# Optimization experiments

Measured on AMD Instinct MI355X. Metric: run time of the kernel, lower is better.

Reference implementation:

```python
import jax, jax.numpy as jnp
import numpy as np

IN_F, OUT_F, USER_F = 1024, 512, 512
BSZ, S = 64, 256


def setup_inputs() -> dict:
    key = jax.random.key(0)
    k = jax.random.split(key, 7)
    X_doc = jax.random.normal(k[0], (BSZ, S, IN_F), dtype=jnp.float32)
    X_user = jax.random.normal(k[1], (BSZ, S, USER_F), dtype=jnp.float32)
    # xavier-normal-ish scaling for weights
    Wd = jax.random.normal(k[2], (OUT_F, IN_F), dtype=jnp.float32) * np.sqrt(2.0 / (IN_F + OUT_F))
    bd = jnp.zeros((OUT_F,), dtype=jnp.float32)
    Wu = jax.random.normal(k[3], (OUT_F, USER_F), dtype=jnp.float32) * np.sqrt(2.0 / (USER_F + OUT_F))
    bu = jnp.zeros((OUT_F,), dtype=jnp.float32)
    W = jax.random.normal(k[4], (OUT_F, OUT_F), dtype=jnp.float32) * np.sqrt(1.0 / OUT_F)
    return {"X_doc": X_doc, "X_user": X_user, "Wd": Wd, "bd": bd, "Wu": Wu, "bu": bu, "W": W}


def reference(X_doc, X_user, Wd, bd, Wu, bu, W):
    d = jnp.einsum('bsi,oi->bso', X_doc, Wd) + bd          # (b, s, out)
    u = jnp.einsum('bsi,oi->bso', X_user, Wu) + bu          # (b, s, out)
    d = d * jax.nn.sigmoid(u)
    u = u * jax.nn.sigmoid(d)
    att = jnp.tanh(jnp.einsum('bsd,de,bre->bsr', d, W, u))  # (b, s, s)
    score_d = jax.nn.softmax(att.mean(axis=2), axis=1)[..., None]  # (b, s, 1)
    score_u = jax.nn.softmax(att.mean(axis=1), axis=1)[..., None]  # (b, s, 1)
    attention_d = jnp.sum(score_d * d, axis=1)              # (b, out)
    attention_u = jnp.sum(score_u * u, axis=1)              # (b, out)
    return (attention_d, attention_u)
```

## Files before the change

kernel.cpp:

```cpp
#include <hip/hip_runtime.h>
#include <hip/hip_bf16.h>

#define S_ 256
#define BSZ_ 64
#define IN_F_ 1024
#define OUT_F_ 512
#define USER_F_ 512

typedef short short8 __attribute__((ext_vector_type(8)));
typedef float f32x4 __attribute__((ext_vector_type(4)));

__device__ __forceinline__ ushort f2bf(float f) {
  unsigned u = __float_as_uint(f);
  unsigned r = (u + 0x7FFFu + ((u >> 16) & 1u)) >> 16;
  return (ushort)r;
}
__device__ __forceinline__ float bf2f(unsigned hi16) {
  return __uint_as_float(hi16 << 16);
}
__device__ __forceinline__ float sigf(float x) {
  return 1.f / (1.f + __expf(-x));
}
__device__ __forceinline__ float tanh_safe(float x) {
  float ax = fabsf(x);
  float e = __expf(-2.f * ax);
  float r = (1.f - e) / (1.f + e);
  return copysignf(r, x);
}

__device__ __forceinline__ void gl_lds16(const ushort* g, ushort* l) {
  __builtin_amdgcn_global_load_lds(
      (const __attribute__((address_space(1))) void*)g,
      (__attribute__((address_space(3))) void*)l, 16, 0, 0);
}

__global__ void prep(const float* __restrict__ Xd, const float* __restrict__ Xu,
                     const float* __restrict__ Wd, const float* __restrict__ Wu,
                     const float* __restrict__ W,
                     ushort* __restrict__ Xd_bf, ushort* __restrict__ Xu_bf,
                     ushort* __restrict__ Wd_bf, ushort* __restrict__ Wu_bf,
                     ushort* __restrict__ Wt_bf, float* __restrict__ rowlog) {
  int i = blockIdx.x * 256 + threadIdx.x;
  if (i < 4194304) {
    float4 v = ((const float4*)Xd)[i];
    ushort4 o; o.x = f2bf(v.x); o.y = f2bf(v.y); o.z = f2bf(v.z); o.w = f2bf(v.w);
    ((ushort4*)Xd_bf)[i] = o;
  } else if (i < 6291456) {
    int j = i - 4194304;
    float4 v = ((const float4*)Xu)[j];
    ushort4 o; o.x = f2bf(v.x); o.y = f2bf(v.y); o.z = f2bf(v.z); o.w = f2bf(v.w);
    ((ushort4*)Xu_bf)[j] = o;
  } else if (i < 6422528) {
    int j = i - 6291456;
    float4 v = ((const float4*)Wd)[j];
    ushort4 o; o.x = f2bf(v.x); o.y = f2bf(v.y); o.z = f2bf(v.z); o.w = f2bf(v.w);
    ((ushort4*)Wd_bf)[j] = o;
  } else if (i < 6488064) {
    int j = i - 6422528;
    float4 v = ((const float4*)Wu)[j];
    ushort4 o; o.x = f2bf(v.x); o.y = f2bf(v.y); o.z = f2bf(v.z); o.w = f2bf(v.w);
    ((ushort4*)Wu_bf)[j] = o;
  } else if (i < 6750208) {
    int j = i - 6488064;
    Wt_bf[j] = f2bf(W[(j & 511) * 512 + (j >> 9)]);
  } else {
    int j = i - 6750208;
    ((float4*)rowlog)[j] = float4{0.f, 0.f, 0.f, 0.f};
  }
}

template <int ROWS>
__device__ __forceinline__ void stage_tile(const ushort* __restrict__ g, int K,
                                           ushort* lds, int w, int lane) {
  const int rin = lane >> 3;
  const int c = lane & 7;
#pragma unroll
  for (int i = 0; i < ROWS / 32; ++i) {
    int r = w * (ROWS / 4) + i * 8 + rin;
    int gc = c ^ (r & 7);
    gl_lds16(g + (long)r * K + gc * 8, lds + w * (ROWS / 4) * 64 + i * 512);
  }
}
__device__ __forceinline__ void stage_tile32(const ushort* __restrict__ g, int K,
                                             ushort* lds, int w, int lane) {
  const int rin = lane >> 3, c = lane & 7;
  int r = w * 8 + rin;
  int gc = c ^ (r & 7);
  gl_lds16(g + (long)r * K + gc * 8, lds + w * 512);
}

__device__ __forceinline__ short8 frag(const ushort* lds, int row, int kk, int q) {
  int pc = (kk * 4 + q) ^ (row & 7);
  return *(const short8*)(lds + row * 64 + pc * 8);
}
__device__ __forceinline__ short8 frag512(const ushort* lds, int row, int k,
                                          int kk, int q) {
  int pc = (kk * 4 + q) ^ (row & 7);
  return *(const short8*)(lds + row * 512 + k * 64 + pc * 8);
}

__device__ __forceinline__ void compute_step(const ushort* As, const ushort* Bs,
                                             f32x4 acc[2][4], int wr, int wc,
                                             int mlane, int q) {
#pragma unroll
  for (int kk = 0; kk < 2; ++kk) {
    short8 af[2], bfr[4];
#pragma unroll
    for (int r = 0; r < 2; ++r) af[r] = frag(As, wr * 32 + r * 16 + mlane, kk, q);
#pragma unroll
    for (int c = 0; c < 4; ++c) bfr[c] = frag(Bs, wc * 64 + c * 16 + mlane, kk, q);
#pragma unroll
    for (int r = 0; r < 2; ++r)
#pragma unroll
      for (int c = 0; c < 4; ++c)
        acc[r][c] = __builtin_amdgcn_mfma_f32_16x16x32_bf16(af[r], bfr[c], acc[r][c], 0, 0, 0);
  }
}

template <int NSTEP>
__device__ __forceinline__ void gemm_loop(const ushort* __restrict__ A,
                                          const ushort* __restrict__ B, int K,
                                          ushort* As, ushort* Bs, f32x4 acc[2][4],
                                          int w, int lane, int wr, int wc,
                                          int mlane, int q) {
#pragma unroll 1
  for (int k = 0; k < NSTEP; ++k) {
    stage_tile<64>(A + k * 64, K, As, w, lane);
    stage_tile<128>(B + k * 64, K, Bs, w, lane);
    __syncthreads();
    compute_step(As, Bs, acc, wr, wc, mlane, q);
    __syncthreads();
  }
}

#define ACC_ZERO(a)                             \
  _Pragma("unroll") for (int r = 0; r < 2; ++r) \
  _Pragma("unroll") for (int c = 0; c < 4; ++c) { \
    a[r][c][0] = 0.f; a[r][c][1] = 0.f; a[r][c][2] = 0.f; a[r][c][3] = 0.f; }

__global__ __launch_bounds__(256, 4) void gemm_du(
    const ushort* __restrict__ Xd, const ushort* __restrict__ Wd,
    const float* __restrict__ bd,
    const ushort* __restrict__ Xu, const ushort* __restrict__ Wu,
    const float* __restrict__ bu,
    ushort* __restrict__ dg, ushort* __restrict__ ug) {
  __shared__ ushort sm[12288];
  ushort* As = sm; ushort* Bs = sm + 4096;
  const int i = blockIdx.x;
  const int k8 = i & 7, j = i >> 3;
  const int by = k8 * 32 + (j >> 2), bx = j & 3;
  const int tid = threadIdx.x, lane = tid & 63, w = tid >> 6;
  const int wr = w >> 1, wc = w & 1, mlane = lane & 15, q = lane >> 4;
  const int m0 = by * 64, n0 = bx * 128;

  f32x4 accd[2][4]; ACC_ZERO(accd);
  gemm_loop<16>(Xd + (long)m0 * 1024, Wd + (long)n0 * 1024, 1024,
                As, Bs, accd, w, lane, wr, wc, mlane, q);
  f32x4 accu[2][4]; ACC_ZERO(accu);
  gemm_loop<8>(Xu + (long)m0 * 512, Wu + (long)n0 * 512, 512,
               As, Bs, accu, w, lane, wr, wc, mlane, q);

#pragma unroll
  for (int c = 0; c < 4; ++c) {
    const int gn = n0 + wc * 64 + c * 16 + mlane;
    const float bdv = bd[gn], buv = bu[gn];
#pragma unroll
    for (int r = 0; r < 2; ++r)
#pragma unroll
      for (int ii = 0; ii < 4; ++ii) {
        const int gm = m0 + wr * 32 + r * 16 + q * 4 + ii;
        const long idx = (long)gm * OUT_F_ + gn;
        float dp = accd[r][c][ii] + bdv;
        float up = accu[r][c][ii] + buv;
        float dgv = dp * sigf(up);
        float ugv = up * sigf(dgv);
        dg[idx] = f2bf(dgv);
        ug[idx] = f2bf(ugv);
      }
  }
}

__global__ __launch_bounds__(256, 2) void gemm_tatt(
    const ushort* __restrict__ dg, const ushort* __restrict__ Wt,
    const ushort* __restrict__ ug, float* __restrict__ rowlog,
    float* __restrict__ collog) {
  __shared__ ushort sm[32768];
  ushort* t_lds = sm;
  ushort* AsT = sm + 16384;
  ushort* BsT = sm + 18432;
  ushort* BsU = sm + 16384;
  const int i = blockIdx.x;
  const int xcd = i & 7, j = i >> 3;
  const int b = xcd * 8 + (j >> 3);
  const int by = j & 7;
  const int tid = threadIdx.x, lane = tid & 63, w = tid >> 6;
  const int mlane = lane & 15, q = lane >> 4;
  const ushort* dgs = dg + (long)b * (S_ * OUT_F_) + (long)by * 32 * 512;
  const ushort* ugb = ug + (long)b * (S_ * OUT_F_);

#pragma unroll 1
  for (int nc = 0; nc < 4; ++nc) {
    f32x4 acc[2][2];
#pragma unroll
    for (int r = 0; r < 2; ++r)
#pragma unroll
      for (int c = 0; c < 2; ++c) {
        acc[r][c][0] = 0.f; acc[r][c][1] = 0.f; acc[r][c][2] = 0.f; acc[r][c][3] = 0.f;
      }
    const ushort* Bw = Wt + (long)(nc * 128) * 512;
#pragma unroll 1
    for (int k = 0; k < 8; ++k) {
      stage_tile32(dgs + k * 64, 512, AsT, w, lane);
      stage_tile<128>(Bw + k * 64, 512, BsT, w, lane);
      __syncthreads();
#pragma unroll
      for (int kk = 0; kk < 2; ++kk) {
        short8 af[2], bfr[2];
#pragma unroll
        for (int r = 0; r < 2; ++r) af[r] = frag(AsT, r * 16 + mlane, kk, q);
#pragma unroll
        for (int c = 0; c < 2; ++c)
          bfr[c] = frag(BsT, w * 32 + c * 16 + mlane, kk, q);
#pragma unroll
        for (int r = 0; r < 2; ++r)
#pragma unroll
          for (int c = 0; c < 2; ++c)
            acc[r][c] = __builtin_amdgcn_mfma_f32_16x16x32_bf16(af[r], bfr[c], acc[r][c], 0, 0, 0);
      }
      __syncthreads();
    }
#pragma unroll
    for (int r = 0; r < 2; ++r)
#pragma unroll
      for (int c = 0; c < 2; ++c)
#pragma unroll
        for (int ii = 0; ii < 4; ++ii) {
          int rr = r * 16 + q * 4 + ii;
          int col = nc * 128 + w * 32 + c * 16 + mlane;
          int cc = col >> 3;
          int ph = (cc & ~7) | ((cc & 7) ^ (rr & 7));
          t_lds[rr * 512 + ph * 8 + (col & 7)] = f2bf(acc[r][c][ii]);
        }
  }

  f32x4 acc[2][4]; ACC_ZERO(acc);
#pragma unroll 1
  for (int k = 0; k < 8; ++k) {
    stage_tile<256>(ugb + k * 64, 512, BsU, w, lane);
    __syncthreads();
#pragma unroll
    for (int kk = 0; kk < 2; ++kk) {
      short8 af[2], bfr[4];
#pragma unroll
      for (int r = 0; r < 2; ++r) af[r] = frag512(t_lds, r * 16 + mlane, k, kk, q);
#pragma unroll
      for (int c = 0; c < 4; ++c)
        bfr[c] = frag(BsU, w * 64 + c * 16 + mlane, kk, q);
#pragma unroll
      for (int r = 0; r < 2; ++r)
#pragma unroll
        for (int c = 0; c < 4; ++c)
          acc[r][c] = __builtin_amdgcn_mfma_f32_16x16x32_bf16(af[r], bfr[c], acc[r][c], 0, 0, 0);
    }
    __syncthreads();
  }

  float rs[8], cs[4];
#pragma unroll
  for (int x = 0; x < 8; ++x) rs[x] = 0.f;
#pragma unroll
  for (int c = 0; c < 4; ++c) cs[c] = 0.f;
#pragma unroll
  for (int r = 0; r < 2; ++r)
#pragma unroll
    for (int c = 0; c < 4; ++c)
#pragma unroll
      for (int ii = 0; ii < 4; ++ii) {
        float v = tanh_safe(acc[r][c][ii]);
        rs[r * 4 + ii] += v;
        cs[c] += v;
      }
#pragma unroll
  for (int m = 1; m < 16; m <<= 1)
#pragma unroll
    for (int x = 0; x < 8; ++x) rs[x] += __shfl_xor(rs[x], m, 64);
#pragma unroll
  for (int m = 16; m < 64; m <<= 1)
#pragma unroll
    for (int c = 0; c < 4; ++c) cs[c] += __shfl_xor(cs[c], m, 64);

  float* rsum = (float*)BsU;
  if (tid < 32) rsum[tid] = 0.f;
  __syncthreads();
  if (mlane == 0) {
#pragma unroll
    for (int x = 0; x < 8; ++x)
      atomicAdd(&rsum[(x >> 2) * 16 + q * 4 + (x & 3)], rs[x]);
  }
  if (q == 0) {
#pragma unroll
    for (int c = 0; c < 4; ++c)
      atomicAdd(&collog[b * S_ + w * 64 + c * 16 + mlane], cs[c]);
  }
  __syncthreads();
  if (tid < 32) rowlog[b * S_ + by * 32 + tid] = rsum[tid];
}

__device__ __forceinline__ float block_max(float v, float* buf, int tid) {
  buf[tid] = v; __syncthreads();
  for (int s = 128; s > 0; s >>= 1) {
    if (tid < s) buf[tid] = fmaxf(buf[tid], buf[tid + s]);
    __syncthreads();
  }
  float r = buf[0]; __syncthreads();
  return r;
}
__device__ __forceinline__ float block_sum(float v, float* buf, int tid) {
  buf[tid] = v; __syncthreads();
  for (int s = 128; s > 0; s >>= 1) {
    if (tid < s) buf[tid] = buf[tid] + buf[tid + s];
    __syncthreads();
  }
  float r = buf[0]; __syncthreads();
  return r;
}

__global__ __launch_bounds__(256) void finalize(
    const float* __restrict__ rowlog, const float* __restrict__ collog,
    const ushort* __restrict__ dg, const ushort* __restrict__ ug,
    float* __restrict__ out) {
  __shared__ float sd[S_], su[S_], buf[S_];
  const int b = blockIdx.x >> 2, oc = blockIdx.x & 3;
  const int tid = threadIdx.x;

  const float rowmean = rowlog[b * S_ + tid] * (1.f / (float)S_);
  const float colmean = collog[b * S_ + tid] * (1.f / (float)S_);

  float md = block_max(rowmean, buf, tid);
  float ed = __expf(rowmean - md);
  float sds = block_sum(ed, buf, tid);
  sd[tid] = ed / sds;
  float mu = block_max(colmean, buf, tid);
  float eu = __expf(colmean - mu);
  float sus = block_sum(eu, buf, tid);
  su[tid] = eu / sus;
  __syncthreads();

  const int o = oc * 128 + (tid & 127);
  const ushort* src = (tid < 128) ? dg : ug;
  const float* sw = (tid < 128) ? sd : su;
  const ushort* p = src + (long)b * (S_ * OUT_F_) + o;
  float a = 0.f;
  for (int s = 0; s < S_; ++s) a += sw[s] * bf2f((unsigned)p[s * OUT_F_]);
  out[((tid < 128) ? 0 : BSZ_ * OUT_F_) + b * OUT_F_ + o] = a;
}

extern "C" void kernel_launch(void* const* d_in, const int* in_sizes, int n_in,
                              void* d_out, int out_size, void* d_ws, size_t ws_size,
                              hipStream_t stream) {
  (void)in_sizes; (void)n_in; (void)out_size; (void)ws_size;
  const float* Xd = (const float*)d_in[0];
  const float* Xu = (const float*)d_in[1];
  const float* Wd = (const float*)d_in[2];
  const float* bd = (const float*)d_in[3];
  const float* Wu = (const float*)d_in[4];
  const float* bu = (const float*)d_in[5];
  const float* W  = (const float*)d_in[6];
  float* out = (float*)d_out;
  char* ws = (char*)d_ws;

  ushort* Xd_bf  = (ushort*)(ws + 0L);
  ushort* Xu_bf  = (ushort*)(ws + 33554432L);
  ushort* Wd_bf  = (ushort*)(ws + 50331648L);
  ushort* Wu_bf  = (ushort*)(ws + 51380224L);
  ushort* Wt_bf  = (ushort*)(ws + 51904512L);
  ushort* dg     = (ushort*)(ws + 52428800L);
  ushort* ug     = (ushort*)(ws + 69206016L);
  float*  rowlog = (float*)(ws + 85983232L);
  float*  collog = (float*)(ws + 86048768L);

  prep<<<26400, 256, 0, stream>>>(Xd, Xu, Wd, Wu, W, Xd_bf, Xu_bf,
                                  Wd_bf, Wu_bf, Wt_bf, rowlog);

  dim3 blk(256);
  gemm_du<<<1024, blk, 0, stream>>>(Xd_bf, Wd_bf, bd, Xu_bf, Wu_bf, bu, dg, ug);
  gemm_tatt<<<512, blk, 0, stream>>>(dg, Wt_bf, ug, rowlog, collog);
  finalize<<<256, 256, 0, stream>>>(rowlog, collog, dg, ug, out);
}
```

Before: 224.5 us.

## Split fused attention GEMM into batched T=dW and T·U kernels with larger tiles

```diff
diff --git a/kernel.cpp b/kernel.cpp
--- a/kernel.cpp
+++ b/kernel.cpp
@@ -81,94 +81,113 @@
     gl_lds16(g + (long)r * K + gc * 8, lds + w * (ROWS / 4) * 64 + i * 512);
   }
 }
-__device__ __forceinline__ void stage_tile32(const ushort* __restrict__ g, int K,
+__device__ __forceinline__ void stage_tile8w(const ushort* __restrict__ g, int K,
                                              ushort* lds, int w, int lane) {
   const int rin = lane >> 3, c = lane & 7;
-  int r = w * 8 + rin;
-  int gc = c ^ (r & 7);
-  gl_lds16(g + (long)r * K + gc * 8, lds + w * 512);
+#pragma unroll
+  for (int i = 0; i < 2; ++i) {
+    int r = w * 16 + i * 8 + rin;
+    int gc = c ^ (r & 7);
+    gl_lds16(g + (long)r * K + gc * 8, lds + w * 1024 + i * 512);
+  }
 }
 
 __device__ __forceinline__ short8 frag(const ushort* lds, int row, int kk, int q) {
   int pc = (kk * 4 + q) ^ (row & 7);
   return *(const short8*)(lds + row * 64 + pc * 8);
 }
-__device__ __forceinline__ short8 frag512(const ushort* lds, int row, int k,
-                                          int kk, int q) {
-  int pc = (kk * 4 + q) ^ (row & 7);
-  return *(const short8*)(lds + row * 512 + k * 64 + pc * 8);
-}
-
-__device__ __forceinline__ void compute_step(const ushort* As, const ushort* Bs,
-                                             f32x4 acc[2][4], int wr, int wc,
-                                             int mlane, int q) {
+
+__device__ __forceinline__ void compute8w(const ushort* As, const ushort* Bs,
+                                          f32x4 acc[4][2], int wr, int wc,
+                                          int mlane, int q) {
 #pragma unroll
   for (int kk = 0; kk < 2; ++kk) {
-    short8 af[2], bfr[4];
-#pragma unroll
-    for (int r = 0; r < 2; ++r) af[r] = frag(As, wr * 32 + r * 16 + mlane, kk, q);
+    short8 af[4], bfr[2];
+#pragma unroll
+    for (int r = 0; r < 4; ++r) af[r] = frag(As, wr * 64 + r * 16 + mlane, kk, q);
+#pragma unroll
+    for (int c = 0; c < 2; ++c) bfr[c] = frag(Bs, wc * 32 + c * 16 + mlane, kk, q);
+#pragma unroll
+    for (int r = 0; r < 4; ++r)
+#pragma unroll
+      for (int c = 0; c < 2; ++c)
+        acc[r][c] = __builtin_amdgcn_mfma_f32_16x16x32_bf16(af[r], bfr[c], acc[r][c], 0, 0, 0);
+  }
+}
+__device__ __forceinline__ void compute4w(const ushort* As, const ushort* Bs,
+                                          f32x4 acc[4][4], int wr, int wc,
+                                          int mlane, int q) {
+#pragma unroll
+  for (int kk = 0; kk < 2; ++kk) {
+    short8 af[4], bfr[4];
+#pragma unroll
+    for (int r = 0; r < 4; ++r) af[r] = frag(As, wr * 64 + r * 16 + mlane, kk, q);
 #pragma unroll
     for (int c = 0; c < 4; ++c) bfr[c] = frag(Bs, wc * 64 + c * 16 + mlane, kk, q);
 #pragma unroll
-    for (int r = 0; r < 2; ++r)
+    for (int r = 0; r < 4; ++r)
 #pragma unroll
       for (int c = 0; c < 4; ++c)
         acc[r][c] = __builtin_amdgcn_mfma_f32_16x16x32_bf16(af[r], bfr[c], acc[r][c], 0, 0, 0);
   }
 }
 
-template <int NSTEP>
-__device__ __forceinline__ void gemm_loop(const ushort* __restrict__ A,
-                                          const ushort* __restrict__ B, int K,
-                                          ushort* As, ushort* Bs, f32x4 acc[2][4],
-                                          int w, int lane, int wr, int wc,
-                                          int mlane, int q) {
-#pragma unroll 1
-  for (int k = 0; k < NSTEP; ++k) {
-    stage_tile<64>(A + k * 64, K, As, w, lane);
-    stage_tile<128>(B + k * 64, K, Bs, w, lane);
-    __syncthreads();
-    compute_step(As, Bs, acc, wr, wc, mlane, q);
-    __syncthreads();
-  }
-}
-
-#define ACC_ZERO(a)                             \
-  _Pragma("unroll") for (int r = 0; r < 2; ++r) \
+#define ACC_ZERO2(a)                            \
+  _Pragma("unroll") for (int r = 0; r < 4; ++r) \
+  _Pragma("unroll") for (int c = 0; c < 2; ++c) { \
+    a[r][c][0] = 0.f; a[r][c][1] = 0.f; a[r][c][2] = 0.f; a[r][c][3] = 0.f; }
+#define ACC_ZERO4(a)                            \
+  _Pragma("unroll") for (int r = 0; r < 4; ++r) \
   _Pragma("unroll") for (int c = 0; c < 4; ++c) { \
     a[r][c][0] = 0.f; a[r][c][1] = 0.f; a[r][c][2] = 0.f; a[r][c][3] = 0.f; }
 
-__global__ __launch_bounds__(256, 4) void gemm_du(
+__global__ __launch_bounds__(512, 4) void gemm_du(
     const ushort* __restrict__ Xd, const ushort* __restrict__ Wd,
     const float* __restrict__ bd,
     const ushort* __restrict__ Xu, const ushort* __restrict__ Wu,
     const float* __restrict__ bu,
     ushort* __restrict__ dg, ushort* __restrict__ ug) {
-  __shared__ ushort sm[12288];
-  ushort* As = sm; ushort* Bs = sm + 4096;
+  __shared__ ushort sm[16384];
+  ushort* As = sm; ushort* Bs = sm + 8192;
   const int i = blockIdx.x;
-  const int k8 = i & 7, j = i >> 3;
-  const int by = k8 * 32 + (j >> 2), bx = j & 3;
+  const int xcd = i & 7, j = i >> 3;
+  const int by = xcd * 16 + (j >> 2), bx = j & 3;
   const int tid = threadIdx.x, lane = tid & 63, w = tid >> 6;
-  const int wr = w >> 1, wc = w & 1, mlane = lane & 15, q = lane >> 4;
-  const int m0 = by * 64, n0 = bx * 128;
-
-  f32x4 accd[2][4]; ACC_ZERO(accd);
-  gemm_loop<16>(Xd + (long)m0 * 1024, Wd + (long)n0 * 1024, 1024,
-                As, Bs, accd, w, lane, wr, wc, mlane, q);
-  f32x4 accu[2][4]; ACC_ZERO(accu);
-  gemm_loop<8>(Xu + (long)m0 * 512, Wu + (long)n0 * 512, 512,
-               As, Bs, accu, w, lane, wr, wc, mlane, q);
-
-#pragma unroll
-  for (int c = 0; c < 4; ++c) {
-    const int gn = n0 + wc * 64 + c * 16 + mlane;
+  const int wr = w >> 2, wc = w & 3, mlane = lane & 15, q = lane >> 4;
+  const int m0 = by * 128, n0 = bx * 128;
+
+  f32x4 accd[4][2]; ACC_ZERO2(accd);
+  const ushort* Ad = Xd + (long)m0 * 1024;
+  const ushort* Bd = Wd + (long)n0 * 1024;
+#pragma unroll 1
+  for (int k = 0; k < 16; ++k) {
+    stage_tile8w(Ad + k * 64, 1024, As, w, lane);
+    stage_tile8w(Bd + k * 64, 1024, Bs, w, lane);
+    __syncthreads();
+    compute8w(As, Bs, accd, wr, wc, mlane, q);
+    __syncthreads();
+  }
+  f32x4 accu[4][2]; ACC_ZERO2(accu);
+  const ushort* Au = Xu + (long)m0 * 512;
+  const ushort* Bu = Wu + (long)n0 * 512;
+#pragma unroll 1
+  for (int k = 0; k < 8; ++k) {
+    stage_tile8w(Au + k * 64, 512, As, w, lane);
+    stage_tile8w(Bu + k * 64, 512, Bs, w, lane);
+    __syncthreads();
+    compute8w(As, Bs, accu, wr, wc, mlane, q);
+    __syncthreads();
+  }
+
+#pragma unroll
+  for (int c = 0; c < 2; ++c) {
+    const int gn = n0 + wc * 32 + c * 16 + mlane;
     const float bdv = bd[gn], buv = bu[gn];
 #pragma unroll
-    for (int r = 0; r < 2; ++r)
+    for (int r = 0; r < 4; ++r)
 #pragma unroll
       for (int ii = 0; ii < 4; ++ii) {
-        const int gm = m0 + wr * 32 + r * 16 + q * 4 + ii;
+        const int gm = m0 + wr * 64 + r * 16 + q * 4 + ii;
         const long idx = (long)gm * OUT_F_ + gn;
         float dp = accd[r][c][ii] + bdv;
         float up = accu[r][c][ii] + buv;
@@ -180,98 +199,73 @@
   }
 }
 
-__global__ __launch_bounds__(256, 2) void gemm_tatt(
+__global__ __launch_bounds__(256, 3) void gemm_t(
     const ushort* __restrict__ dg, const ushort* __restrict__ Wt,
-    const ushort* __restrict__ ug, float* __restrict__ rowlog,
-    float* __restrict__ collog) {
-  __shared__ ushort sm[32768];
-  ushort* t_lds = sm;
-  ushort* AsT = sm + 16384;
-  ushort* BsT = sm + 18432;
-  ushort* BsU = sm + 16384;
+    ushort* __restrict__ t) {
+  __shared__ ushort sm[16384];
+  ushort* As = sm; ushort* Bs = sm + 8192;
   const int i = blockIdx.x;
   const int xcd = i & 7, j = i >> 3;
-  const int b = xcd * 8 + (j >> 3);
-  const int by = j & 7;
+  const int by = xcd * 16 + (j >> 2), bx = j & 3;
   const int tid = threadIdx.x, lane = tid & 63, w = tid >> 6;
-  const int mlane = lane & 15, q = lane >> 4;
-  const ushort* dgs = dg + (long)b * (S_ * OUT_F_) + (long)by * 32 * 512;
-  const ushort* ugb = ug + (long)b * (S_ * OUT_F_);
-
-#pragma unroll 1
-  for (int nc = 0; nc < 4; ++nc) {
-    f32x4 acc[2][2];
-#pragma unroll
-    for (int r = 0; r < 2; ++r)
-#pragma unroll
-      for (int c = 0; c < 2; ++c) {
-        acc[r][c][0] = 0.f; acc[r][c][1] = 0.f; acc[r][c][2] = 0.f; acc[r][c][3] = 0.f;
-      }
-    const ushort* Bw = Wt + (long)(nc * 128) * 512;
-#pragma unroll 1
-    for (int k = 0; k < 8; ++k) {
-      stage_tile32(dgs + k * 64, 512, AsT, w, lane);
-      stage_tile<128>(Bw + k * 64, 512, BsT, w, lane);
-      __syncthreads();
-#pragma unroll
-      for (int kk = 0; kk < 2; ++kk) {
-        short8 af[2], bfr[2];
-#pragma unroll
-        for (int r = 0; r < 2; ++r) af[r] = frag(AsT, r * 16 + mlane, kk, q);
-#pragma unroll
-        for (int c = 0; c < 2; ++c)
-          bfr[c] = frag(BsT, w * 32 + c * 16 + mlane, kk, q);
-#pragma unroll
-        for (int r = 0; r < 2; ++r)
-#pragma unroll
-          for (int c = 0; c < 2; ++c)
-            acc[r][c] = __builtin_amdgcn_mfma_f32_16x16x32_bf16(af[r], bfr[c], acc[r][c], 0, 0, 0);
-      }
-      __syncthreads();
-    }
-#pragma unroll
-    for (int r = 0; r < 2; ++r)
-#pragma unroll
-      for (int c = 0; c < 2; ++c)
-#pragma unroll
-        for (int ii = 0; ii < 4; ++ii) {
-          int rr = r * 16 + q * 4 + ii;
-          int col = nc * 128 + w * 32 + c * 16 + mlane;
-          int cc = col >> 3;
-          int ph = (cc & ~7) | ((cc & 7) ^ (rr & 7));
-          t_lds[rr * 512 + ph * 8 + (col & 7)] = f2bf(acc[r][c][ii]);
-        }
-  }
-
-  f32x4 acc[2][4]; ACC_ZERO(acc);
+  const int wr = w >> 1, wc = w & 1, mlane = lane & 15, q = lane >> 4;
+  const int m0 = by * 128, n0 = bx * 128;
+
+  f32x4 acc[4][4]; ACC_ZERO4(acc);
+  const ushort* A = dg + (long)m0 * 512;
+  const ushort* B = Wt + (long)n0 * 512;
 #pragma unroll 1
   for (int k = 0; k < 8; ++k) {
-    stage_tile<256>(ugb + k * 64, 512, BsU, w, lane);
-    __syncthreads();
-#pragma unroll
-    for (int kk = 0; kk < 2; ++kk) {
-      short8 af[2], bfr[4];
-#pragma unroll
-      for (int r = 0; r < 2; ++r) af[r] = frag512(t_lds, r * 16 + mlane, k, kk, q);
-#pragma unroll
-      for (int c = 0; c < 4; ++c)
-        bfr[c] = frag(BsU, w * 64 + c * 16 + mlane, kk, q);
-#pragma unroll
-      for (int r = 0; r < 2; ++r)
-#pragma unroll
-        for (int c = 0; c < 4; ++c)
-          acc[r][c] = __builtin_amdgcn_mfma_f32_16x16x32_bf16(af[r], bfr[c], acc[r][c], 0, 0, 0);
-    }
-    __syncthreads();
-  }
-
-  float rs[8], cs[4];
-#pragma unroll
-  for (int x = 0; x < 8; ++x) rs[x] = 0.f;
+    stage_tile<128>(A + k * 64, 512, As, w, lane);
+    stage_tile<128>(B + k * 64, 512, Bs, w, lane);
+    __syncthreads();
+    compute4w(As, Bs, acc, wr, wc, mlane, q);
+    __syncthreads();
+  }
+#pragma unroll
+  for (int c = 0; c < 4; ++c) {
+    const int gn = n0 + wc * 64 + c * 16 + mlane;
+#pragma unroll
+    for (int r = 0; r < 4; ++r)
+#pragma unroll
+      for (int ii = 0; ii < 4; ++ii) {
+        const int gm = m0 + wr * 64 + r * 16 + q * 4 + ii;
+        t[(long)gm * OUT_F_ + gn] = f2bf(acc[r][c][ii]);
+      }
+  }
+}
+
+__global__ __launch_bounds__(256, 3) void att(
+    const ushort* __restrict__ t, const ushort* __restrict__ ug,
+    float* __restrict__ rowlog, float* __restrict__ collog) {
+  __shared__ ushort sm[16384];
+  ushort* As = sm; ushort* Bs = sm + 8192;
+  const int i = blockIdx.x;
+  const int xcd = i & 7, j = i >> 3;
+  const int b = xcd * 8 + (j >> 2);
+  const int mt = (j >> 1) & 1, nt = j & 1;
+  const int tid = threadIdx.x, lane = tid & 63, w = tid >> 6;
+  const int wr = w >> 1, wc = w & 1, mlane = lane & 15, q = lane >> 4;
+
+  f32x4 acc[4][4]; ACC_ZERO4(acc);
+  const ushort* A = t + ((long)b * S_ + mt * 128) * 512;
+  const ushort* B = ug + ((long)b * S_ + nt * 128) * 512;
+#pragma unroll 1
+  for (int k = 0; k < 8; ++k) {
+    stage_tile<128>(A + k * 64, 512, As, w, lane);
+    stage_tile<128>(B + k * 64, 512, Bs, w, lane);
+    __syncthreads();
+    compute4w(As, Bs, acc, wr, wc, mlane, q);
+    __syncthreads();
+  }
+
+  float rs[16], cs[4];
+#pragma unroll
+  for (int x = 0; x < 16; ++x) rs[x] = 0.f;
 #pragma unroll
   for (int c = 0; c < 4; ++c) cs[c] = 0.f;
 #pragma unroll
-  for (int r = 0; r < 2; ++r)
+  for (int r = 0; r < 4; ++r)
 #pragma unroll
     for (int c = 0; c < 4; ++c)
 #pragma unroll
@@ -283,27 +277,24 @@
 #pragma unroll
   for (int m = 1; m < 16; m <<= 1)
 #pragma unroll
-    for (int x = 0; x < 8; ++x) rs[x] += __shfl_xor(rs[x], m, 64);
+    for (int x = 0; x < 16; ++x) rs[x] += __shfl_xor(rs[x], m, 64);
 #pragma unroll
   for (int m = 16; m < 64; m <<= 1)
 #pragma unroll
     for (int c = 0; c < 4; ++c) cs[c] += __shfl_xor(cs[c], m, 64);
 
-  float* rsum = (float*)BsU;
-  if (tid < 32) rsum[tid] = 0.f;
-  __syncthreads();
+  const int s0 = mt * 128 + wr * 64;
+  const int r0 = nt * 128 + wc * 64;
   if (mlane == 0) {
 #pragma unroll
-    for (int x = 0; x < 8; ++x)
-      atomicAdd(&rsum[(x >> 2) * 16 + q * 4 + (x & 3)], rs[x]);
+    for (int x = 0; x < 16; ++x)
+      atomicAdd(&rowlog[b * S_ + s0 + (x >> 2) * 16 + q * 4 + (x & 3)], rs[x]);
   }
   if (q == 0) {
 #pragma unroll
     for (int c = 0; c < 4; ++c)
-      atomicAdd(&collog[b * S_ + w * 64 + c * 16 + mlane], cs[c]);
-  }
-  __syncthreads();
-  if (tid < 32) rowlog[b * S_ + by * 32 + tid] = rsum[tid];
+      atomicAdd(&collog[b * S_ + r0 + c * 16 + mlane], cs[c]);
+  }
 }
 
 __device__ __forceinline__ float block_max(float v, float* buf, int tid) {
@@ -351,6 +342,7 @@
   const float* sw = (tid < 128) ? sd : su;
   const ushort* p = src + (long)b * (S_ * OUT_F_) + o;
   float a = 0.f;
+#pragma unroll 8
   for (int s = 0; s < S_; ++s) a += sw[s] * bf2f((unsigned)p[s * OUT_F_]);
   out[((tid < 128) ? 0 : BSZ_ * OUT_F_) + b * OUT_F_ + o] = a;
 }
@@ -378,12 +370,13 @@
   ushort* ug     = (ushort*)(ws + 69206016L);
   float*  rowlog = (float*)(ws + 85983232L);
   float*  collog = (float*)(ws + 86048768L);
+  ushort* t_buf  = Xd_bf;
 
   prep<<<26400, 256, 0, stream>>>(Xd, Xu, Wd, Wu, W, Xd_bf, Xu_bf,
                                   Wd_bf, Wu_bf, Wt_bf, rowlog);
 
-  dim3 blk(256);
-  gemm_du<<<1024, blk, 0, stream>>>(Xd_bf, Wd_bf, bd, Xu_bf, Wu_bf, bu, dg, ug);
-  gemm_tatt<<<512, blk, 0, stream>>>(dg, Wt_bf, ug, rowlog, collog);
-  finalize<<<256, 256, 0, stream>>>(rowlog, collog, dg, ug, out);
-}
+  gemm_du<<<512, dim3(512), 0, stream>>>(Xd_bf, Wd_bf, bd, Xu_bf, Wu_bf, bu, dg, ug);
+  gemm_t<<<512, dim3(256), 0, stream>>>(dg, Wt_bf, t_buf);
+  att<<<256, dim3(256), 0, stream>>>(t_buf, ug, rowlog, collog);
+  finalize<<<256, dim3(256), 0, stream>>>(rowlog, collog, dg, ug, out);
+}
```

Measured after the change: 213.3 us. 5.0% less time.
